# Optimization experiments

Hardware: AMD Instinct MI355X
Metric: run time of the kernel (lower is better)

The kernel has to match this reference:

```python
import jax, jax.numpy as jnp
import numpy as np

# Grid / physics constants (match init_kwargs)
NX, NY, NZ = 256, 256, 128
LX, LY, LZ = 1.0, 1.0, 1.0
CP, CV, MU, KTH, G = 1004.0, 717.0, 1.8e-5, 0.025, 9.8
DX = LX / NX            # periodic spacing in x
DY = LY / NY            # periodic spacing in y
DZ = LZ / (NZ - 1)      # non-periodic spacing in z


def _d1p(f, axis, d):
    # second-order central first derivative, periodic axis
    return (jnp.roll(f, -1, axis) - jnp.roll(f, 1, axis)) * (0.5 / d)


def _d2p(f, axis, d):
    # second-order central second derivative, periodic axis
    return (jnp.roll(f, -1, axis) + jnp.roll(f, 1, axis) - 2.0 * f) * (1.0 / (d * d))


def _d1z(f, d):
    # non-periodic first derivative along last axis: central interior, 2nd-order one-sided at walls
    inv2d = 0.5 / d
    c = (f[..., 2:] - f[..., :-2]) * inv2d
    lo = (-3.0 * f[..., 0:1] + 4.0 * f[..., 1:2] - f[..., 2:3]) * inv2d
    hi = (3.0 * f[..., -1:] - 4.0 * f[..., -2:-1] + f[..., -3:-2]) * inv2d
    return jnp.concatenate([lo, c, hi], axis=-1)


def _d2z(f, d):
    # non-periodic second derivative along last axis: central interior, 2nd-order one-sided at walls
    invd2 = 1.0 / (d * d)
    c = (f[..., 2:] - 2.0 * f[..., 1:-1] + f[..., :-2]) * invd2
    lo = (2.0 * f[..., 0:1] - 5.0 * f[..., 1:2] + 4.0 * f[..., 2:3] - f[..., 3:4]) * invd2
    hi = (2.0 * f[..., -1:] - 5.0 * f[..., -2:-1] + 4.0 * f[..., -3:-2] - f[..., -4:-3]) * invd2
    return jnp.concatenate([lo, c, hi], axis=-1)


def _lap(f):
    return _d2p(f, 0, DX) + _d2p(f, 1, DY) + _d2z(f, DZ)


def _adv(q, u, v, w):
    # u*dq/dx + v*dq/dy + w*dq/dz
    return u * _d1p(q, 0, DX) + v * _d1p(q, 1, DY) + w * _d1z(q, DZ)


def setup_inputs() -> dict:
    key = jax.random.key(0)
    state = 0.05 * jax.random.normal(key, (6, NX, NY, NZ), dtype=jnp.float32)
    # keep density positive and temperature physical (state order: u,v,w,rou,T,c)
    state = state.at[3].add(1.0)
    state = state.at[4].add(300.0)
    return {"state": state, "t": 0}


def reference(state, t):
    u, v, w, rou, T, c = state  # each [NX, NY, NZ]
    p = (CP - CV) * rou * T

    # NOTE: original code only applies -d/dx(rou*u) to drou; the y/z flux line is a no-op expression.
    drou = -_d1p(rou * u, 0, DX)

    du = (-_d1p(p, 0, DX) + MU * _lap(u)) / rou - _adv(u, u, v, w)
    dv = (-_d1p(p, 1, DY) + MU * _lap(v)) / rou - _adv(v, u, v, w)
    dw = (-G * rou - _d1z(p, DZ) + MU * _lap(w)) / rou - _adv(w, u, v, w)
    dT = KTH * _lap(T) / rou / CV - _adv(T, u, v, w)
    dc = -_adv(c, u, v, w)

    result = jnp.stack([du, dv, dw, drou, dT, dc], axis=0)
    # zero momentum and temperature tendencies at z walls
    result = result.at[0:3, :, :, 0].set(0.0)
    result = result.at[0:3, :, :, -1].set(0.0)
    result = result.at[4, :, :, 0].set(0.0)
    result = result.at[4, :, :, -1].set(0.0)
    return result
```

## Files before the change

### kernel.cpp

```cpp
#include <hip/hip_runtime.h>


namespace {
constexpr int NXc = 256, NYc = 256, NZc = 128;
constexpr int FS = NXc * NYc * NZc;
constexpr int XS = NYc * NZc;
constexpr int YS = NZc;

constexpr float MUc = 1.8e-5f, KTHc = 0.025f, Gc = 9.8f;
constexpr float Rgas = 287.0f;
constexpr float invCV = 1.0f / 717.0f;

constexpr float inv2dx = 128.0f, inv2dy = 128.0f, inv2dz = 63.5f;
constexpr float invdx2 = 65536.0f, invdy2 = 65536.0f, invdz2 = 16129.0f;

constexpr int BY = 4;
constexpr int RPF = BY + 2 + BY + BY;
constexpr int TOT_ROWS = 6 * RPF;
constexpr int ROW_B = NZc * 4;
constexpr int LDS_B = TOT_ROWS * ROW_B;

typedef float nf4 __attribute__((ext_vector_type(4)));
typedef const __attribute__((address_space(1))) unsigned int gu32;
typedef __attribute__((address_space(3))) unsigned int lu32;
}

__device__ __forceinline__ void st_nt(float4 v, float4* p) {
    nf4 nv;
    nv.x = v.x; nv.y = v.y; nv.z = v.z; nv.w = v.w;
    __builtin_nontemporal_store(nv, reinterpret_cast<nf4*>(p));
}

#define LROW(fi, rr) (*(const float4*)(smem + ((fi) * RPF + (rr)) * ROW_B + tx * 16))
#define LOADN(q, fi) \
    const float4 q##_ym = LROW(fi, ty), q##_yp = LROW(fi, 2 + ty); \
    const float4 q##_xm = LROW(fi, 6 + ty), q##_xp = LROW(fi, 10 + ty); \
    const float q##_zm = __shfl_up(q##_c.w, 1, 32); \
    const float q##_zp = __shfl_down(q##_c.x, 1, 32);

#define ADV_LAP_C(q, C, PREV, NEXT) \
    adv_##q.C = u_c.C * (q##_xp.C - q##_xm.C) * inv2dx \
              + v_c.C * (q##_yp.C - q##_ym.C) * inv2dy \
              + w_c.C * ((NEXT) - (PREV)) * inv2dz; \
    lap_##q.C = (q##_xp.C + q##_xm.C - 2.0f * q##_c.C) * invdx2 \
              + (q##_yp.C + q##_ym.C - 2.0f * q##_c.C) * invdy2 \
              + ((NEXT) + (PREV) - 2.0f * q##_c.C) * invdz2;

#define DERIVS(q) \
    float4 adv_##q, lap_##q; \
    ADV_LAP_C(q, x, q##_zm,  q##_c.y) \
    ADV_LAP_C(q, y, q##_c.x, q##_c.z) \
    ADV_LAP_C(q, z, q##_c.y, q##_c.w) \
    ADV_LAP_C(q, w, q##_c.z, q##_zp)

__global__ __launch_bounds__(128) void rb_kernel(const float* __restrict__ s,
                                                 float* __restrict__ o) {
    extern __shared__ char smem[];

    const int tx = threadIdx.x;
    const int ty = threadIdx.y;
    const int ty0 = blockIdx.x * BY;
    const int y = ty0 + ty;
    const int x = blockIdx.y;

    const int xm = (x == 0) ? NXc - 1 : x - 1;
    const int xp = (x == NXc - 1) ? 0 : x + 1;

    {
        const int wid = ty >> 1;
        const int half = ty & 1;
        const char* sb = (const char*)s;
        for (int p = wid; p < TOT_ROWS / 2; p += 2) {
            const int R = 2 * p + half;
            const int f = R / RPF;
            const int rr = R - f * RPF;
            int gx, gy;
            if (rr < BY + 2)      { gx = x;  gy = (ty0 + rr + NYc - 1) & (NYc - 1); }
            else if (rr < 2 * BY + 2) { gx = xm; gy = ty0 + (rr - (BY + 2)); }
            else                  { gx = xp; gy = ty0 + (rr - (2 * BY + 2)); }
            const char* gp = sb + 4u * ((unsigned)f * FS + (unsigned)gx * XS
                                        + (unsigned)gy * YS) + tx * 16;
            __builtin_amdgcn_global_load_lds((gu32*)gp,
                                             (lu32*)(smem + p * 1024),
                                             16, 0, 0);
        }
    }
    __syncthreads();

    const float4 u_c = LROW(0, 1 + ty), v_c = LROW(1, 1 + ty), w_c = LROW(2, 1 + ty);
    const float4 r_c = LROW(3, 1 + ty), T_c = LROW(4, 1 + ty), c_c = LROW(5, 1 + ty);

    float4 inv_r;
    inv_r.x = 1.0f / r_c.x; inv_r.y = 1.0f / r_c.y;
    inv_r.z = 1.0f / r_c.z; inv_r.w = 1.0f / r_c.w;

    LOADN(T, 4)
    DERIVS(T)
    LOADN(r, 3)

    float4 p_c, p_xm, p_xp, p_ym, p_yp;
#define PC(C) \
    p_c.C  = Rgas * r_c.C  * T_c.C; \
    p_xm.C = Rgas * r_xm.C * T_xm.C;  p_xp.C = Rgas * r_xp.C * T_xp.C; \
    p_ym.C = Rgas * r_ym.C * T_ym.C;  p_yp.C = Rgas * r_yp.C * T_yp.C;
    PC(x) PC(y) PC(z) PC(w)
#undef PC
    const float p_zm = __shfl_up(p_c.w, 1, 32);
    const float p_zp = __shfl_down(p_c.x, 1, 32);

    float4 dpdx, dpdy, dpdz;
#define DP(C) \
    dpdx.C = (p_xp.C - p_xm.C) * inv2dx; \
    dpdy.C = (p_yp.C - p_ym.C) * inv2dy;
    DP(x) DP(y) DP(z) DP(w)
#undef DP
    dpdz.x = (p_c.y - p_zm) * inv2dz;
    dpdz.y = (p_c.z - p_c.x) * inv2dz;
    dpdz.z = (p_c.w - p_c.y) * inv2dz;
    dpdz.w = (p_zp  - p_c.z) * inv2dz;

    LOADN(u, 0)
    DERIVS(u)
    float4 drou;
#define DR(C) drou.C = -(r_xp.C * u_xp.C - r_xm.C * u_xm.C) * inv2dx;
    DR(x) DR(y) DR(z) DR(w)
#undef DR

    LOADN(v, 1)
    DERIVS(v)

    LOADN(w, 2)
    DERIVS(w)

    LOADN(c, 5)
    DERIVS(c)
    (void)lap_c;

    float4 du4, dv4, dw4, dT4, dc4;
#define OUT(C) \
    du4.C = (-dpdx.C + MUc * lap_u.C) * inv_r.C - adv_u.C; \
    dv4.C = (-dpdy.C + MUc * lap_v.C) * inv_r.C - adv_v.C; \
    dw4.C = (-Gc * r_c.C - dpdz.C + MUc * lap_w.C) * inv_r.C - adv_w.C; \
    dT4.C = KTHc * lap_T.C * inv_r.C * invCV - adv_T.C; \
    dc4.C = -adv_c.C;
    OUT(x) OUT(y) OUT(z) OUT(w)
#undef OUT

    if (tx == 0) {
        du4.x = 0.0f; dv4.x = 0.0f; dw4.x = 0.0f; dT4.x = 0.0f;
        const float dzc0 = (-3.0f * c_c.x + 4.0f * c_c.y - c_c.z) * inv2dz;
        dc4.x = -(u_c.x * (c_xp.x - c_xm.x) * inv2dx
                + v_c.x * (c_yp.x - c_ym.x) * inv2dy
                + w_c.x * dzc0);
    }
    if (tx == 31) {
        du4.w = 0.0f; dv4.w = 0.0f; dw4.w = 0.0f; dT4.w = 0.0f;
        const float dzcN = (3.0f * c_c.w - 4.0f * c_c.z + c_c.y) * inv2dz;
        dc4.w = -(u_c.w * (c_xp.w - c_xm.w) * inv2dx
                + v_c.w * (c_yp.w - c_ym.w) * inv2dy
                + w_c.w * dzcN);
    }

    const int b4 = (x * XS + y * YS) / 4 + tx;
    float4* o4 = reinterpret_cast<float4*>(o);
    const int fs4 = FS / 4;
    st_nt(du4,  o4 + b4);
    st_nt(dv4,  o4 + b4 + fs4);
    st_nt(dw4,  o4 + b4 + 2 * fs4);
    st_nt(drou, o4 + b4 + 3 * fs4);
    st_nt(dT4,  o4 + b4 + 4 * fs4);
    st_nt(dc4,  o4 + b4 + 5 * fs4);
}

extern "C" void kernel_launch(void* const* d_in, const int* in_sizes, int n_in,
                              void* d_out, int out_size, void* d_ws, size_t ws_size,
                              hipStream_t stream) {
    (void)in_sizes; (void)n_in; (void)d_ws; (void)ws_size; (void)out_size;
    const float* s = (const float*)d_in[0];
    float* o = (float*)d_out;

    dim3 block(32, BY, 1);
    dim3 grid(NYc / BY, NXc, 1);
    rb_kernel<<<grid, block, LDS_B, stream>>>(s, o);
}
```

Before: 365.4 us.

## March blocks along x with a rotating three-plane LDS buffer and prefetch

Each block now marches through 64 consecutive x planes instead of handling one x column. A ring of three LDS plane slots holds x-1, x and x+1 data, the x-1 centre values are kept in registers, and the next plane is prefetched asynchronously while the current one is computed. Stores for each plane are deferred by one iteration. This drops the redundant reloads of the x-neighbour rows, cutting global read traffic, at the cost of far fewer blocks (1024 instead of 16384) and a __syncthreads per plane, which may hurt occupancy and latency hiding.

After: 407.9 us. 11.6% more time.

```diff
diff --git a/kernel.cpp b/kernel.cpp
--- a/kernel.cpp
+++ b/kernel.cpp
@@ -14,11 +14,14 @@
 constexpr float inv2dx = 128.0f, inv2dy = 128.0f, inv2dz = 63.5f;
 constexpr float invdx2 = 65536.0f, invdy2 = 65536.0f, invdz2 = 16129.0f;
 
-constexpr int BY = 4;
-constexpr int RPF = BY + 2 + BY + BY;
-constexpr int TOT_ROWS = 6 * RPF;
+constexpr int BYt = 4;
+constexpr int MARCH = 64;
+constexpr int RPP = BYt + 2;
+constexpr int PLANE_ROWS = 6 * RPP;
 constexpr int ROW_B = NZc * 4;
-constexpr int LDS_B = TOT_ROWS * ROW_B;
+constexpr int PLANE_B = PLANE_ROWS * ROW_B;
+constexpr int NSLOT = 3;
+constexpr int LDS_B = NSLOT * PLANE_B;
 
 typedef float nf4 __attribute__((ext_vector_type(4)));
 typedef const __attribute__((address_space(1))) unsigned int gu32;
@@ -31,18 +34,41 @@
     __builtin_nontemporal_store(nv, reinterpret_cast<nf4*>(p));
 }
 
-#define LROW(fi, rr) (*(const float4*)(smem + ((fi) * RPF + (rr)) * ROW_B + tx * 16))
-#define LOADN(q, fi) \
-    const float4 q##_ym = LROW(fi, ty), q##_yp = LROW(fi, 2 + ty); \
-    const float4 q##_xm = LROW(fi, 6 + ty), q##_xp = LROW(fi, 10 + ty); \
+#define SLOT(q) (((q) + NSLOT) % NSLOT)
+
+__device__ __forceinline__ void stage_plane(const char* __restrict__ sb,
+                                            char* __restrict__ smem,
+                                            int q, int y0, int tx, int ty) {
+    const int w = ty >> 1;
+    const int h = ty & 1;
+    const int gx = q & (NXc - 1);
+    char* lbase = smem + SLOT(q) * PLANE_B;
+    for (int p = w; p < PLANE_ROWS / 2; p += 2) {
+        const int R = 2 * p + h;
+        const int f = R / RPP;
+        const int r = R - f * RPP;
+        const int gy = (y0 + r - 1) & (NYc - 1);
+        const char* gp = sb + 4u * ((unsigned)f * FS + (unsigned)gx * XS
+                                    + (unsigned)gy * YS) + tx * 16;
+        __builtin_amdgcn_global_load_lds((gu32*)gp, (lu32*)(lbase + p * 1024),
+                                         16, 0, 0);
+    }
+}
+
+#define LROW(q, fi, rr) \
+    (*(const float4*)(smem + SLOT(q) * PLANE_B + ((fi) * RPP + (rr)) * ROW_B + tx * 16))
+
+#define NEIGH(q, fi) \
+    const float4 q##_ym = LROW(P,  fi, ty),     q##_yp = LROW(P,  fi, ty + 2); \
+    const float4 q##_xp = LROW(Pp, fi, ty + 1); \
     const float q##_zm = __shfl_up(q##_c.w, 1, 32); \
     const float q##_zp = __shfl_down(q##_c.x, 1, 32);
 
 #define ADV_LAP_C(q, C, PREV, NEXT) \
-    adv_##q.C = u_c.C * (q##_xp.C - q##_xm.C) * inv2dx \
+    adv_##q.C = u_c.C * (q##_xp.C - prev_##q.C) * inv2dx \
               + v_c.C * (q##_yp.C - q##_ym.C) * inv2dy \
               + w_c.C * ((NEXT) - (PREV)) * inv2dz; \
-    lap_##q.C = (q##_xp.C + q##_xm.C - 2.0f * q##_c.C) * invdx2 \
+    lap_##q.C = (q##_xp.C + prev_##q.C - 2.0f * q##_c.C) * invdx2 \
               + (q##_yp.C + q##_ym.C - 2.0f * q##_c.C) * invdy2 \
               + ((NEXT) + (PREV) - 2.0f * q##_c.C) * invdz2;
 
@@ -55,121 +81,137 @@
 
 __global__ __launch_bounds__(128) void rb_kernel(const float* __restrict__ s,
                                                  float* __restrict__ o) {
-    extern __shared__ char smem[];
+    __shared__ char smem[LDS_B];
 
     const int tx = threadIdx.x;
     const int ty = threadIdx.y;
-    const int ty0 = blockIdx.x * BY;
-    const int y = ty0 + ty;
-    const int x = blockIdx.y;
-
-    const int xm = (x == 0) ? NXc - 1 : x - 1;
-    const int xp = (x == NXc - 1) ? 0 : x + 1;
-
-    {
-        const int wid = ty >> 1;
-        const int half = ty & 1;
-        const char* sb = (const char*)s;
-        for (int p = wid; p < TOT_ROWS / 2; p += 2) {
-            const int R = 2 * p + half;
-            const int f = R / RPF;
-            const int rr = R - f * RPF;
-            int gx, gy;
-            if (rr < BY + 2)      { gx = x;  gy = (ty0 + rr + NYc - 1) & (NYc - 1); }
-            else if (rr < 2 * BY + 2) { gx = xm; gy = ty0 + (rr - (BY + 2)); }
-            else                  { gx = xp; gy = ty0 + (rr - (2 * BY + 2)); }
-            const char* gp = sb + 4u * ((unsigned)f * FS + (unsigned)gx * XS
-                                        + (unsigned)gy * YS) + tx * 16;
-            __builtin_amdgcn_global_load_lds((gu32*)gp,
-                                             (lu32*)(smem + p * 1024),
-                                             16, 0, 0);
-        }
-    }
-    __syncthreads();
-
-    const float4 u_c = LROW(0, 1 + ty), v_c = LROW(1, 1 + ty), w_c = LROW(2, 1 + ty);
-    const float4 r_c = LROW(3, 1 + ty), T_c = LROW(4, 1 + ty), c_c = LROW(5, 1 + ty);
-
-    float4 inv_r;
-    inv_r.x = 1.0f / r_c.x; inv_r.y = 1.0f / r_c.y;
-    inv_r.z = 1.0f / r_c.z; inv_r.w = 1.0f / r_c.w;
-
-    LOADN(T, 4)
-    DERIVS(T)
-    LOADN(r, 3)
-
-    float4 p_c, p_xm, p_xp, p_ym, p_yp;
-#define PC(C) \
-    p_c.C  = Rgas * r_c.C  * T_c.C; \
-    p_xm.C = Rgas * r_xm.C * T_xm.C;  p_xp.C = Rgas * r_xp.C * T_xp.C; \
-    p_ym.C = Rgas * r_ym.C * T_ym.C;  p_yp.C = Rgas * r_yp.C * T_yp.C;
-    PC(x) PC(y) PC(z) PC(w)
-#undef PC
-    const float p_zm = __shfl_up(p_c.w, 1, 32);
-    const float p_zp = __shfl_down(p_c.x, 1, 32);
-
-    float4 dpdx, dpdy, dpdz;
-#define DP(C) \
-    dpdx.C = (p_xp.C - p_xm.C) * inv2dx; \
-    dpdy.C = (p_yp.C - p_ym.C) * inv2dy;
-    DP(x) DP(y) DP(z) DP(w)
-#undef DP
-    dpdz.x = (p_c.y - p_zm) * inv2dz;
-    dpdz.y = (p_c.z - p_c.x) * inv2dz;
-    dpdz.z = (p_c.w - p_c.y) * inv2dz;
-    dpdz.w = (p_zp  - p_c.z) * inv2dz;
-
-    LOADN(u, 0)
-    DERIVS(u)
-    float4 drou;
-#define DR(C) drou.C = -(r_xp.C * u_xp.C - r_xm.C * u_xm.C) * inv2dx;
-    DR(x) DR(y) DR(z) DR(w)
-#undef DR
-
-    LOADN(v, 1)
-    DERIVS(v)
-
-    LOADN(w, 2)
-    DERIVS(w)
-
-    LOADN(c, 5)
-    DERIVS(c)
-    (void)lap_c;
-
-    float4 du4, dv4, dw4, dT4, dc4;
-#define OUT(C) \
-    du4.C = (-dpdx.C + MUc * lap_u.C) * inv_r.C - adv_u.C; \
-    dv4.C = (-dpdy.C + MUc * lap_v.C) * inv_r.C - adv_v.C; \
-    dw4.C = (-Gc * r_c.C - dpdz.C + MUc * lap_w.C) * inv_r.C - adv_w.C; \
-    dT4.C = KTHc * lap_T.C * inv_r.C * invCV - adv_T.C; \
-    dc4.C = -adv_c.C;
-    OUT(x) OUT(y) OUT(z) OUT(w)
-#undef OUT
-
-    if (tx == 0) {
-        du4.x = 0.0f; dv4.x = 0.0f; dw4.x = 0.0f; dT4.x = 0.0f;
-        const float dzc0 = (-3.0f * c_c.x + 4.0f * c_c.y - c_c.z) * inv2dz;
-        dc4.x = -(u_c.x * (c_xp.x - c_xm.x) * inv2dx
-                + v_c.x * (c_yp.x - c_ym.x) * inv2dy
-                + w_c.x * dzc0);
-    }
-    if (tx == 31) {
-        du4.w = 0.0f; dv4.w = 0.0f; dw4.w = 0.0f; dT4.w = 0.0f;
-        const float dzcN = (3.0f * c_c.w - 4.0f * c_c.z + c_c.y) * inv2dz;
-        dc4.w = -(u_c.w * (c_xp.w - c_xm.w) * inv2dx
-                + v_c.w * (c_yp.w - c_ym.w) * inv2dy
-                + w_c.w * dzcN);
-    }
-
-    const int b4 = (x * XS + y * YS) / 4 + tx;
+    const int y0 = blockIdx.x * BYt;
+    const int x0 = blockIdx.y * MARCH;
+    const int y = y0 + ty;
+
+    const char* sb = (const char*)s;
     float4* o4 = reinterpret_cast<float4*>(o);
     const int fs4 = FS / 4;
-    st_nt(du4,  o4 + b4);
-    st_nt(dv4,  o4 + b4 + fs4);
-    st_nt(dw4,  o4 + b4 + 2 * fs4);
-    st_nt(drou, o4 + b4 + 3 * fs4);
-    st_nt(dT4,  o4 + b4 + 4 * fs4);
-    st_nt(dc4,  o4 + b4 + 5 * fs4);
+
+    stage_plane(sb, smem, x0 - 1, y0, tx, ty);
+    stage_plane(sb, smem, x0,     y0, tx, ty);
+    stage_plane(sb, smem, x0 + 1, y0, tx, ty);
+    __syncthreads();
+
+    float4 prev_u = LROW(x0 - 1, 0, ty + 1), prev_v = LROW(x0 - 1, 1, ty + 1),
+           prev_w = LROW(x0 - 1, 2, ty + 1), prev_r = LROW(x0 - 1, 3, ty + 1),
+           prev_T = LROW(x0 - 1, 4, ty + 1), prev_c = LROW(x0 - 1, 5, ty + 1);
+    __syncthreads();
+
+    float4 du4, dv4, dw4, drou, dT4, dc4;
+
+#pragma unroll 1
+    for (int i = 0; i < MARCH; ++i) {
+        const int P = x0 + i, Pp = P + 1;
+
+        if (i < MARCH - 1)
+            stage_plane(sb, smem, P + 2, y0, tx, ty);
+
+        if (i > 0) {
+            const int b4p = ((P - 1) * XS + y * YS) / 4 + tx;
+            st_nt(du4,  o4 + b4p);
+            st_nt(dv4,  o4 + b4p + fs4);
+            st_nt(dw4,  o4 + b4p + 2 * fs4);
+            st_nt(drou, o4 + b4p + 3 * fs4);
+            st_nt(dT4,  o4 + b4p + 4 * fs4);
+            st_nt(dc4,  o4 + b4p + 5 * fs4);
+        }
+
+        const float4 u_c = LROW(P, 0, ty + 1), v_c = LROW(P, 1, ty + 1),
+                     w_c = LROW(P, 2, ty + 1), r_c = LROW(P, 3, ty + 1),
+                     T_c = LROW(P, 4, ty + 1), c_c = LROW(P, 5, ty + 1);
+
+        float4 inv_r;
+        inv_r.x = 1.0f / r_c.x; inv_r.y = 1.0f / r_c.y;
+        inv_r.z = 1.0f / r_c.z; inv_r.w = 1.0f / r_c.w;
+
+        NEIGH(T, 4)
+        DERIVS(T)
+        NEIGH(r, 3)
+
+        float4 p_c, p_xm, p_xp, p_ym, p_yp;
+#define PC(C) \
+        p_c.C  = Rgas * r_c.C    * T_c.C; \
+        p_xm.C = Rgas * prev_r.C * prev_T.C; \
+        p_xp.C = Rgas * r_xp.C   * T_xp.C; \
+        p_ym.C = Rgas * r_ym.C   * T_ym.C; \
+        p_yp.C = Rgas * r_yp.C   * T_yp.C;
+        PC(x) PC(y) PC(z) PC(w)
+#undef PC
+        const float p_zm = __shfl_up(p_c.w, 1, 32);
+        const float p_zp = __shfl_down(p_c.x, 1, 32);
+
+        float4 dpdx, dpdy, dpdz;
+#define DP(C) \
+        dpdx.C = (p_xp.C - p_xm.C) * inv2dx; \
+        dpdy.C = (p_yp.C - p_ym.C) * inv2dy;
+        DP(x) DP(y) DP(z) DP(w)
+#undef DP
+        dpdz.x = (p_c.y - p_zm) * inv2dz;
+        dpdz.y = (p_c.z - p_c.x) * inv2dz;
+        dpdz.z = (p_c.w - p_c.y) * inv2dz;
+        dpdz.w = (p_zp  - p_c.z) * inv2dz;
+
+        NEIGH(u, 0)
+        DERIVS(u)
+#define DR(C) drou.C = -(r_xp.C * u_xp.C - prev_r.C * prev_u.C) * inv2dx;
+        DR(x) DR(y) DR(z) DR(w)
+#undef DR
+
+        NEIGH(v, 1)
+        DERIVS(v)
+
+        NEIGH(w, 2)
+        DERIVS(w)
+
+        NEIGH(c, 5)
+        DERIVS(c)
+        (void)lap_c;
+
+#define OUT(C) \
+        du4.C = (-dpdx.C + MUc * lap_u.C) * inv_r.C - adv_u.C; \
+        dv4.C = (-dpdy.C + MUc * lap_v.C) * inv_r.C - adv_v.C; \
+        dw4.C = (-Gc * r_c.C - dpdz.C + MUc * lap_w.C) * inv_r.C - adv_w.C; \
+        dT4.C = KTHc * lap_T.C * inv_r.C * invCV - adv_T.C; \
+        dc4.C = -adv_c.C;
+        OUT(x) OUT(y) OUT(z) OUT(w)
+#undef OUT
+
+        if (tx == 0) {
+            du4.x = 0.0f; dv4.x = 0.0f; dw4.x = 0.0f; dT4.x = 0.0f;
+            const float dzc0 = (-3.0f * c_c.x + 4.0f * c_c.y - c_c.z) * inv2dz;
+            dc4.x = -(u_c.x * (c_xp.x - prev_c.x) * inv2dx
+                    + v_c.x * (c_yp.x - c_ym.x) * inv2dy
+                    + w_c.x * dzc0);
+        }
+        if (tx == 31) {
+            du4.w = 0.0f; dv4.w = 0.0f; dw4.w = 0.0f; dT4.w = 0.0f;
+            const float dzcN = (3.0f * c_c.w - 4.0f * c_c.z + c_c.y) * inv2dz;
+            dc4.w = -(u_c.w * (c_xp.w - prev_c.w) * inv2dx
+                    + v_c.w * (c_yp.w - c_ym.w) * inv2dy
+                    + w_c.w * dzcN);
+        }
+
+        prev_u = u_c; prev_v = v_c; prev_w = w_c;
+        prev_r = r_c; prev_T = T_c; prev_c = c_c;
+
+        __syncthreads();
+    }
+
+    {
+        const int b4p = ((x0 + MARCH - 1) * XS + y * YS) / 4 + tx;
+        st_nt(du4,  o4 + b4p);
+        st_nt(dv4,  o4 + b4p + fs4);
+        st_nt(dw4,  o4 + b4p + 2 * fs4);
+        st_nt(drou, o4 + b4p + 3 * fs4);
+        st_nt(dT4,  o4 + b4p + 4 * fs4);
+        st_nt(dc4,  o4 + b4p + 5 * fs4);
+    }
 }
 
 extern "C" void kernel_launch(void* const* d_in, const int* in_sizes, int n_in,
@@ -179,7 +221,7 @@
     const float* s = (const float*)d_in[0];
     float* o = (float*)d_out;
 
-    dim3 block(32, BY, 1);
-    dim3 grid(NYc / BY, NXc, 1);
-    rb_kernel<<<grid, block, LDS_B, stream>>>(s, o);
-}
+    dim3 block(32, BYt, 1);
+    dim3 grid(NYc / BYt, NXc / MARCH, 1);
+    rb_kernel<<<grid, block, 0, stream>>>(s, o);
+}
```
